# Performance work log

Hardware: AMD Instinct MI355X
Metric: run time of the kernel (lower is better)

The kernel has to match this reference:

```python
import jax, jax.numpy as jnp
import numpy as np

NH = 16  # num_heads from init_kwargs


def setup_inputs() -> dict:
    key = jax.random.key(0)
    ks = jax.random.split(key, 7)
    B, L, S, H = 4, 2, 1024, 1024
    s = 0.02  # weight init scale to keep logits numerically tame
    return {
        "x": jax.random.normal(ks[0], (B, S, H), jnp.float32),
        "y": jax.random.normal(ks[1], (L, B, S, H), jnp.float32),
        "bias": jax.random.normal(ks[2], (B, 1, 1, S), jnp.float32),
        "Wq": jax.random.normal(ks[3], (H, H), jnp.float32) * s,
        "Wk": jax.random.normal(ks[4], (L, H, H), jnp.float32) * s,
        "Wv": jax.random.normal(ks[5], (L, H, H), jnp.float32) * s,
        "Wo": jax.random.normal(ks[6], (H, H), jnp.float32) * s,
    }


def reference(x, y, bias, Wq, Wk, Wv, Wo):
    # x: [B, Lq, H]; y: [L, B, Lk, H] (stacked list of per-link memories)
    B, Lq, H = x.shape
    L, _, Lk, _ = y.shape
    d = H // NH

    # shared query projection, split heads: [B, NH, Lq, d], pre-scaled
    q = (x @ Wq).reshape(B, Lq, NH, d).transpose(0, 2, 1, 3) * (d ** -0.5)

    # per-link K/V projections, split heads -> [B, L, NH, Lk, d]
    kp = jnp.einsum('lbsh,lhe->lbse', y, Wk).reshape(L, B, Lk, NH, d).transpose(1, 0, 3, 2, 4)
    vp = jnp.einsum('lbsh,lhe->lbse', y, Wv).reshape(L, B, Lk, NH, d).transpose(1, 0, 3, 2, 4)

    # per-link logits [B, L, NH, Lq, Lk] + broadcast bias (concat across links == broadcast)
    logits = jnp.einsum('bhqd,blhkd->blhqk', q, kp) + bias[:, None]

    # computation_mode == 1: joint softmax over the link-summed logits
    joint = logits.sum(axis=1)                # [B, NH, Lq, Lk]
    w = jax.nn.softmax(joint, axis=-1)        # (training=False -> no dropout)

    # sum_l (w @ v_l) == w @ sum_l v_l  (w is shared across links)
    ctx = jnp.einsum('bhqk,bhkd->bhqd', w, vp.sum(axis=1))

    # combine heads [B, Lq, H] and output projection
    out = ctx.transpose(0, 2, 1, 3).reshape(B, Lq, H) @ Wo
    return out
```

## Files before the change

kernel.cpp:

```cpp
#include <hip/hip_runtime.h>
#include <cstdint>

typedef __bf16 bf16_t;
typedef bf16_t bf16x4 __attribute__((ext_vector_type(4)));
typedef bf16_t bf16x8 __attribute__((ext_vector_type(8)));
typedef float f32x4 __attribute__((ext_vector_type(4)));
typedef float f32x16 __attribute__((ext_vector_type(16)));

#define GLD_LDS16(g, l)                                                        \
  __builtin_amdgcn_global_load_lds(                                            \
      (const __attribute__((address_space(1))) void*)(g),                      \
      (__attribute__((address_space(3))) void*)(l), 16, 0, 0)

#define LOG2E 1.44269504088896340736f

static __device__ __forceinline__ unsigned short bf16_bits(float f) {
  bf16_t h = (bf16_t)f;
  return __builtin_bit_cast(unsigned short, h);
}

__global__ void prep_kernel(const float* __restrict__ x,
                            const float* __restrict__ y,
                            const float* __restrict__ Wq,
                            const float* __restrict__ Wk,
                            const float* __restrict__ Wv,
                            const float* __restrict__ Wo,
                            bf16_t* __restrict__ xb, bf16_t* __restrict__ yb,
                            bf16_t* __restrict__ WqT,
                            bf16_t* __restrict__ WkvT,
                            bf16_t* __restrict__ WoT) {
  __shared__ float tile[32][33];
  int bid = blockIdx.x;
  if (bid < 6144) {
    int i = bid * 256 + threadIdx.x;
    const float* src;
    bf16_t* dst;
    if (i < 524288) { src = x; dst = xb; }
    else            { src = y; dst = yb; i -= 524288; }
    const float4* s = (const float4*)src;
    float4 a = s[i * 2];
    float4 b = s[i * 2 + 1];
    bf16x8 o;
    o[0] = (bf16_t)a.x; o[1] = (bf16_t)a.y; o[2] = (bf16_t)a.z; o[3] = (bf16_t)a.w;
    o[4] = (bf16_t)b.x; o[5] = (bf16_t)b.y; o[6] = (bf16_t)b.z; o[7] = (bf16_t)b.w;
    *(bf16x8*)(dst + (size_t)i * 8) = o;
    return;
  }
  bid -= 6144;
  const float* src; bf16_t* dst; int R, lb;
  if (bid < 1024)      { src = Wq; dst = WqT;                        R = 1024; lb = bid; }
  else if (bid < 3072) { src = Wk; dst = WkvT;                       R = 2048; lb = bid - 1024; }
  else if (bid < 5120) { src = Wv; dst = WkvT + (size_t)1024 * 2048; R = 2048; lb = bid - 3072; }
  else                 { src = Wo; dst = WoT;                        R = 1024; lb = bid - 5120; }
  int c0 = (lb & 31) << 5, r0 = (lb >> 5) << 5;
  int tc = threadIdx.x & 31, tr = threadIdx.x >> 5;
#pragma unroll
  for (int i = 0; i < 4; i++)
    tile[tr + i * 8][tc] = src[(size_t)(r0 + tr + i * 8) * 1024 + c0 + tc];
  __syncthreads();
#pragma unroll
  for (int i = 0; i < 4; i++)
    dst[(size_t)(c0 + tr + i * 8) * R + r0 + tc] = (bf16_t)tile[tc][tr + i * 8];
}

#define GEMM_STAGE(buf, kt)                                                    \
  {                                                                            \
    const int kbase = (kt) * 32;                                               \
    int kg0 = kbase + ak0;                                                     \
    const bf16_t* s0 = (kg0 < Ksplit)                                          \
                           ? (A0 + (size_t)(m0 + ar0) * 1024 + kg0)            \
                           : (A1 + (size_t)(m0 + ar0) * 1024 + (kg0 - Ksplit));\
    GLD_LDS16(s0, As[buf] + c0 * 8);                                           \
    int kg1 = kbase + ak1;                                                     \
    const bf16_t* s1 = (kg1 < Ksplit)                                          \
                           ? (A0 + (size_t)(m0 + ar1) * 1024 + kg1)            \
                           : (A1 + (size_t)(m0 + ar1) * 1024 + (kg1 - Ksplit));\
    GLD_LDS16(s1, As[buf] + c1 * 8);                                           \
    const bf16_t* b0 = BT + (size_t)(n0 + ar0) * Ktot + kbase + ak0;           \
    GLD_LDS16(b0, Bs[buf] + c0 * 8);                                           \
    const bf16_t* b1 = BT + (size_t)(n0 + ar1) * Ktot + kbase + ak1;           \
    GLD_LDS16(b1, Bs[buf] + c1 * 8);                                           \
  }

#define GEMM_DECLS                                                             \
  const int t = threadIdx.x, w = t >> 6, l = t & 63;                           \
  const int l15 = l & 15, l4 = l >> 4;                                         \
  const int wr = w >> 1, wc = w & 1;                                           \
  const int c0 = t, c1 = t + 256;                                              \
  const int ar0 = c0 >> 2, ar1 = c1 >> 2;                                      \
  const int ak0 = ((c0 & 3) ^ ((ar0 >> 1) & 3)) * 8;                           \
  const int ak1 = ((c1 & 3) ^ ((ar1 >> 1) & 3)) * 8;                           \
  int offA[4], offB[4];                                                        \
  _Pragma("unroll") for (int mi = 0; mi < 4; mi++) {                           \
    int rA = wr * 64 + mi * 16 + l15;                                          \
    offA[mi] = rA * 32 + (l4 ^ ((rA >> 1) & 3)) * 8;                           \
    int rB = wc * 64 + mi * 16 + l15;                                          \
    offB[mi] = rB * 32 + (l4 ^ ((rB >> 1) & 3)) * 8;                           \
  }

#define GEMM_MAINLOOP                                                          \
  GEMM_STAGE(0, 0);                                                            \
  __syncthreads();                                                             \
  int cur = 0;                                                                 \
  for (int kt = 0; kt < nkt; ++kt) {                                           \
    if (kt + 1 < nkt) GEMM_STAGE(cur ^ 1, kt + 1);                             \
    bf16x8 af[4], bfr[4];                                                      \
    _Pragma("unroll") for (int mi = 0; mi < 4; mi++)                           \
        af[mi] = *(const bf16x8*)&As[cur][offA[mi]];                           \
    _Pragma("unroll") for (int ni = 0; ni < 4; ni++)                           \
        bfr[ni] = *(const bf16x8*)&Bs[cur][offB[ni]];                          \
    _Pragma("unroll") for (int mi = 0; mi < 4; mi++)                           \
        _Pragma("unroll") for (int ni = 0; ni < 4; ni++)                       \
            acc[mi][ni] = __builtin_amdgcn_mfma_f32_16x16x32_bf16(             \
                af[mi], bfr[ni], acc[mi][ni], 0, 0, 0);                        \
    __syncthreads();                                                           \
    cur ^= 1;                                                                  \
  }

__global__ __launch_bounds__(256, 2) void qkv_kernel(
    const bf16_t* __restrict__ xbp, const bf16_t* __restrict__ ybp,
    const bf16_t* __restrict__ WqT, const bf16_t* __restrict__ WkvT,
    bf16_t* __restrict__ Qb, bf16_t* __restrict__ Kb,
    bf16_t* __restrict__ VTb) {
  __shared__ bf16_t As[2][128 * 32];
  __shared__ bf16_t Bs[2][128 * 32];
  GEMM_DECLS
  const bool isQ = blockIdx.x < 256;
  const int i = isQ ? blockIdx.x : blockIdx.x - 256;
  const int ybt = (i & 7) * 4 + ((i >> 3) & 3);
  const int xbt = i >> 5;
  const int m0 = ybt * 128, n0 = xbt * 128;
  const bf16_t* A0 = isQ ? xbp : ybp;
  const bf16_t* A1 = isQ ? xbp : ybp + (size_t)4096 * 1024;
  const int Ksplit = 1024;
  const bf16_t* BT = isQ ? WqT : WkvT;
  const int Ktot = isQ ? 1024 : 2048;
  const int nkt = Ktot >> 5;
  f32x4 acc[4][4] = {};

  GEMM_MAINLOOP

#pragma unroll
  for (int mi = 0; mi < 4; mi++) {
#pragma unroll
    for (int ni = 0; ni < 4; ni++) {
      const int rbase = m0 + wr * 64 + mi * 16 + l4 * 4;
      const int col = n0 + wc * 64 + ni * 16 + l15;
      if (isQ) {
#pragma unroll
        for (int rr = 0; rr < 4; rr++)
          Qb[(size_t)(rbase + rr) * 1024 + col] =
              (bf16_t)(acc[mi][ni][rr] * (0.125f * LOG2E));
      } else if (n0 < 1024) {
#pragma unroll
        for (int rr = 0; rr < 4; rr++)
          Kb[(size_t)(rbase + rr) * 1024 + col] = (bf16_t)acc[mi][ni][rr];
      } else {
        union { unsigned short u[4]; uint2 v; } pk;
#pragma unroll
        for (int rr = 0; rr < 4; rr++)
          pk.u[rr] = bf16_bits(acc[mi][ni][rr]);
        *(uint2*)&VTb[(size_t)(col - 1024) * 4096 + rbase] = pk.v;
      }
    }
  }
}

__global__ __launch_bounds__(256, 2) void gemm_o(const bf16_t* __restrict__ A0,
                                                 const bf16_t* __restrict__ BT,
                                                 float* __restrict__ Cp) {
  __shared__ bf16_t As[2][128 * 32];
  __shared__ bf16_t Bs[2][64 * 32];
  const int t = threadIdx.x, w = t >> 6, l = t & 63;
  const int l15 = l & 15, l4 = l >> 4;
  const int wr = w >> 1, wc = w & 1;
  const int c0 = t, c1 = t + 256, c2 = t;
  const int ar0 = c0 >> 2, ar1 = c1 >> 2, br2 = c2 >> 2;
  const int ak0 = ((c0 & 3) ^ ((ar0 >> 1) & 3)) * 8;
  const int ak1 = ((c1 & 3) ^ ((ar1 >> 1) & 3)) * 8;
  const int bk2 = ((c2 & 3) ^ ((br2 >> 1) & 3)) * 8;
  int offA[4], offB[2];
#pragma unroll
  for (int mi = 0; mi < 4; mi++) {
    int rA = wr * 64 + mi * 16 + l15;
    offA[mi] = rA * 32 + (l4 ^ ((rA >> 1) & 3)) * 8;
  }
#pragma unroll
  for (int ni = 0; ni < 2; ni++) {
    int rB = wc * 32 + ni * 16 + l15;
    offB[ni] = rB * 32 + (l4 ^ ((rB >> 1) & 3)) * 8;
  }
  const int i = blockIdx.x;
  const int ybt = (i & 7) * 4 + ((i >> 3) & 3);
  const int xbt = i >> 5;
  const int m0 = ybt * 128, n0 = xbt * 64;
  const int nkt = 32;
  f32x4 acc[4][2] = {};

#define OST(buf, kt)                                                           \
  {                                                                            \
    const int kbase = (kt) * 32;                                               \
    const bf16_t* s0 = A0 + (size_t)(m0 + ar0) * 1024 + kbase + ak0;           \
    GLD_LDS16(s0, As[buf] + c0 * 8);                                           \
    const bf16_t* s1 = A0 + (size_t)(m0 + ar1) * 1024 + kbase + ak1;           \
    GLD_LDS16(s1, As[buf] + c1 * 8);                                           \
    const bf16_t* b0 = BT + (size_t)(n0 + br2) * 1024 + kbase + bk2;           \
    GLD_LDS16(b0, Bs[buf] + c2 * 8);                                           \
  }

  OST(0, 0);
  __syncthreads();
  int cur = 0;
  for (int kt = 0; kt < nkt; ++kt) {
    if (kt + 1 < nkt) OST(cur ^ 1, kt + 1);
    bf16x8 af[4], bfr[2];
#pragma unroll
    for (int mi = 0; mi < 4; mi++)
      af[mi] = *(const bf16x8*)&As[cur][offA[mi]];
#pragma unroll
    for (int ni = 0; ni < 2; ni++)
      bfr[ni] = *(const bf16x8*)&Bs[cur][offB[ni]];
#pragma unroll
    for (int mi = 0; mi < 4; mi++)
#pragma unroll
      for (int ni = 0; ni < 2; ni++)
        acc[mi][ni] = __builtin_amdgcn_mfma_f32_16x16x32_bf16(
            af[mi], bfr[ni], acc[mi][ni], 0, 0, 0);
    __syncthreads();
    cur ^= 1;
  }
#undef OST

#pragma unroll
  for (int mi = 0; mi < 4; mi++) {
#pragma unroll
    for (int ni = 0; ni < 2; ni++) {
      const int rbase = m0 + wr * 64 + mi * 16 + l4 * 4;
      const int col = n0 + wc * 32 + ni * 16 + l15;
#pragma unroll
      for (int rr = 0; rr < 4; rr++)
        Cp[(size_t)(rbase + rr) * 1024 + col] = acc[mi][ni][rr];
    }
  }
}

__global__ __launch_bounds__(256, 2) void attn_kernel(
    const bf16_t* __restrict__ Q, const bf16_t* __restrict__ K,
    const bf16_t* __restrict__ VT, const float* __restrict__ bias,
    bf16_t* __restrict__ ctx) {
  __shared__ bf16_t Ks[2][128 * 64];
  __shared__ bf16_t Vs[2][64 * 128];
  const int t = threadIdx.x, w = t >> 6, l = t & 63;
  const int l31 = l & 31, hi = l >> 5;
  const int id = blockIdx.x;
  const int bh = id & 63, qt = id >> 6;
  const int b = bh >> 4, h = bh & 15;
  const int q_local = w * 32 + l31;

  bf16x8 qf[4];
  {
    const bf16_t* Qp =
        Q + (size_t)(b * 1024 + qt * 128 + q_local) * 1024 + h * 64 + hi * 8;
#pragma unroll
    for (int ds = 0; ds < 4; ds++) qf[ds] = *(const bf16x8*)&Qp[ds * 16];
  }

#define ATTN_STAGE(buf, kt)                                                    \
  {                                                                            \
    _Pragma("unroll") for (int j = 0; j < 4; j++) {                            \
      int c = t + j * 256;                                                     \
      int rowk = c >> 3, slk = (c & 7) ^ (rowk & 7);                           \
      const bf16_t* srck =                                                     \
          K + (size_t)(b * 1024 + (kt) * 128 + rowk) * 1024 + h * 64 + slk * 8;\
      GLD_LDS16(srck, Ks[buf] + c * 8);                                        \
      int rowv = c >> 4, slv = (c & 15) ^ ((rowv & 7) << 1);                   \
      const bf16_t* srcv =                                                     \
          VT + (size_t)(h * 64 + rowv) * 4096 + b * 1024 + (kt) * 128 +        \
          slv * 8;                                                             \
      GLD_LDS16(srcv, Vs[buf] + c * 8);                                        \
    }                                                                          \
  }

  float mrun = -INFINITY, lrun = 0.f;
  f32x16 cacc[2] = {};

  ATTN_STAGE(0, 0);
  __syncthreads();
  int cur = 0;
  for (int kts = 0; kts < 8; ++kts) {
    if (kts + 1 < 8) ATTN_STAGE(cur ^ 1, kts + 1);

#pragma unroll
    for (int half = 0; half < 2; ++half) {
      f32x16 sacc[2] = {};
#pragma unroll
      for (int ds = 0; ds < 4; ds++) {
#pragma unroll
        for (int kg = 0; kg < 2; kg++) {
          int krow = half * 64 + kg * 32 + l31;
          int eoff = krow * 64 + (((ds * 2 + hi) ^ (krow & 7)) * 8);
          bf16x8 kf = *(const bf16x8*)&Ks[cur][eoff];
          sacc[kg] = __builtin_amdgcn_mfma_f32_32x32x16_bf16(
              kf, qf[ds], sacc[kg], 0, 0, 0);
        }
      }
#pragma unroll
      for (int kg = 0; kg < 2; kg++) {
#pragma unroll
        for (int mm = 0; mm < 4; mm++) {
          f32x4 bb = *(const f32x4*)&bias[b * 1024 + kts * 128 + half * 64 +
                                          kg * 32 + mm * 8 + hi * 4];
#pragma unroll
          for (int rr = 0; rr < 4; rr++)
            sacc[kg][mm * 4 + rr] += (2.0f * LOG2E) * bb[rr];
        }
      }
      float tm = -INFINITY;
#pragma unroll
      for (int kg = 0; kg < 2; kg++)
#pragma unroll
        for (int r = 0; r < 16; r++) tm = fmaxf(tm, sacc[kg][r]);
      tm = fmaxf(tm, __shfl_xor(tm, 32));
      float mnew = fmaxf(mrun, tm);
      float sc = exp2f(mrun - mnew);
      float rsum = 0.f;
#pragma unroll
      for (int kg = 0; kg < 2; kg++)
#pragma unroll
        for (int r = 0; r < 16; r++) {
          float p = exp2f(sacc[kg][r] - mnew);
          sacc[kg][r] = p;
          rsum += p;
        }
      rsum += __shfl_xor(rsum, 32);
      lrun = lrun * sc + rsum;
      mrun = mnew;
#pragma unroll
      for (int dg = 0; dg < 2; dg++)
#pragma unroll
        for (int r = 0; r < 16; r++) cacc[dg][r] *= sc;

      bf16x8 pb[4];
#pragma unroll
      for (int kg = 0; kg < 2; kg++) {
#pragma unroll
        for (int tt = 0; tt < 2; tt++) {
          uint32_t w0A, w1A, w0B, w1B;
          const int mA = 2 * tt, mB = 2 * tt + 1;
          asm("v_cvt_pk_bf16_f32 %0, %1, %2"
              : "=v"(w0A)
              : "v"(sacc[kg][4 * mA + 0]), "v"(sacc[kg][4 * mA + 1]));
          asm("v_cvt_pk_bf16_f32 %0, %1, %2"
              : "=v"(w1A)
              : "v"(sacc[kg][4 * mA + 2]), "v"(sacc[kg][4 * mA + 3]));
          asm("v_cvt_pk_bf16_f32 %0, %1, %2"
              : "=v"(w0B)
              : "v"(sacc[kg][4 * mB + 0]), "v"(sacc[kg][4 * mB + 1]));
          asm("v_cvt_pk_bf16_f32 %0, %1, %2"
              : "=v"(w1B)
              : "v"(sacc[kg][4 * mB + 2]), "v"(sacc[kg][4 * mB + 3]));
          asm("v_permlane32_swap_b32 %0, %1" : "+v"(w0A), "+v"(w0B));
          asm("v_permlane32_swap_b32 %0, %1" : "+v"(w1A), "+v"(w1B));
          union { uint32_t u[4]; bf16x8 v; } pk;
          pk.u[0] = w0A; pk.u[1] = w1A; pk.u[2] = w0B; pk.u[3] = w1B;
          pb[kg * 2 + tt] = pk.v;
        }
      }
#pragma unroll
      for (int dg = 0; dg < 2; dg++) {
#pragma unroll
        for (int k4 = 0; k4 < 4; k4++) {
          int vrow = dg * 32 + l31;
          int s = half * 8 + k4 * 2 + hi;
          int eoff = vrow * 128 + ((s ^ ((vrow & 7) << 1)) * 8);
          bf16x8 vf = *(const bf16x8*)&Vs[cur][eoff];
          cacc[dg] = __builtin_amdgcn_mfma_f32_32x32x16_bf16(
              vf, pb[k4], cacc[dg], 0, 0, 0);
        }
      }
    }
    __syncthreads();
    cur ^= 1;
  }

  bf16_t* T = (bf16_t*)Ks;
  {
    float inv = 1.0f / lrun;
#pragma unroll
    for (int dg = 0; dg < 2; dg++) {
#pragma unroll
      for (int m = 0; m < 4; m++) {
        bf16x4 tv;
#pragma unroll
        for (int rr = 0; rr < 4; rr++)
          tv[rr] = (bf16_t)(cacc[dg][4 * m + rr] * inv);
        int d0 = dg * 32 + m * 8 + hi * 4;
        *(bf16x4*)&T[q_local * 64 + (d0 ^ ((q_local & 7) << 3))] = tv;
      }
    }
  }
  __syncthreads();
#pragma unroll
  for (int c = t; c < 1024; c += 256) {
    int row = c >> 3, col8 = c & 7;
    bf16x8 v = *(const bf16x8*)&T[row * 64 + ((col8 * 8) ^ ((row & 7) << 3))];
    *(bf16x8*)&ctx[(size_t)(b * 1024 + qt * 128 + row) * 1024 + h * 64 +
                   col8 * 8] = v;
  }
#undef ATTN_STAGE
}

extern "C" void kernel_launch(void* const* d_in, const int* in_sizes, int n_in,
                              void* d_out, int out_size, void* d_ws,
                              size_t ws_size, hipStream_t stream) {
  const float* x = (const float*)d_in[0];
  const float* y = (const float*)d_in[1];
  const float* bias = (const float*)d_in[2];
  const float* Wq = (const float*)d_in[3];
  const float* Wk = (const float*)d_in[4];
  const float* Wv = (const float*)d_in[5];
  const float* Wo = (const float*)d_in[6];
  float* out = (float*)d_out;

  char* ws = (char*)d_ws;
  const size_t MB = 1024 * 1024;
  bf16_t* xb   = (bf16_t*)(ws + 0 * MB);
  bf16_t* yb   = (bf16_t*)(ws + 8 * MB);
  bf16_t* WqT  = (bf16_t*)(ws + 24 * MB);
  bf16_t* WkvT = (bf16_t*)(ws + 26 * MB);
  bf16_t* WoT  = (bf16_t*)(ws + 34 * MB);
  bf16_t* Qb   = (bf16_t*)(ws + 36 * MB);
  bf16_t* Kb   = (bf16_t*)(ws + 44 * MB);
  bf16_t* VTb  = (bf16_t*)(ws + 52 * MB);
  bf16_t* ctxb = (bf16_t*)(ws + 60 * MB);

  prep_kernel<<<12288, 256, 0, stream>>>(x, y, Wq, Wk, Wv, Wo, xb, yb, WqT,
                                         WkvT, WoT);
  qkv_kernel<<<768, 256, 0, stream>>>(xb, yb, WqT, WkvT, Qb, Kb, VTb);
  attn_kernel<<<512, 256, 0, stream>>>(Qb, Kb, VTb, bias, ctxb);
  gemm_o<<<512, 256, 0, stream>>>(ctxb, WoT, out);
}
```

Before: 134.3 us.

## Fuse fp32-to-bf16 activation conversion into QKV GEMM A-operand loads

Removes the separate pass that converts x and y from fp32 to bf16. The QKV GEMM now reads fp32 activations straight into registers, converts them, and writes them into swizzled LDS, with a register-staged prefetch of the next k-tile. The block order is also changed so the K/V blocks launch before the Q blocks. This avoids writing and rereading roughly 24MB of bf16 intermediates, at the cost of twice the global A-operand bytes inside the GEMM and a full vmcnt(0) wait each iteration that may limit overlap.

```diff
diff --git a/kernel.cpp b/kernel.cpp
--- a/kernel.cpp
+++ b/kernel.cpp
@@ -19,34 +19,15 @@
   return __builtin_bit_cast(unsigned short, h);
 }
 
-__global__ void prep_kernel(const float* __restrict__ x,
-                            const float* __restrict__ y,
-                            const float* __restrict__ Wq,
+__global__ void prep_kernel(const float* __restrict__ Wq,
                             const float* __restrict__ Wk,
                             const float* __restrict__ Wv,
                             const float* __restrict__ Wo,
-                            bf16_t* __restrict__ xb, bf16_t* __restrict__ yb,
                             bf16_t* __restrict__ WqT,
                             bf16_t* __restrict__ WkvT,
                             bf16_t* __restrict__ WoT) {
   __shared__ float tile[32][33];
   int bid = blockIdx.x;
-  if (bid < 6144) {
-    int i = bid * 256 + threadIdx.x;
-    const float* src;
-    bf16_t* dst;
-    if (i < 524288) { src = x; dst = xb; }
-    else            { src = y; dst = yb; i -= 524288; }
-    const float4* s = (const float4*)src;
-    float4 a = s[i * 2];
-    float4 b = s[i * 2 + 1];
-    bf16x8 o;
-    o[0] = (bf16_t)a.x; o[1] = (bf16_t)a.y; o[2] = (bf16_t)a.z; o[3] = (bf16_t)a.w;
-    o[4] = (bf16_t)b.x; o[5] = (bf16_t)b.y; o[6] = (bf16_t)b.z; o[7] = (bf16_t)b.w;
-    *(bf16x8*)(dst + (size_t)i * 8) = o;
-    return;
-  }
-  bid -= 6144;
   const float* src; bf16_t* dst; int R, lb;
   if (bid < 1024)      { src = Wq; dst = WqT;                        R = 1024; lb = bid; }
   else if (bid < 3072) { src = Wk; dst = WkvT;                       R = 2048; lb = bid - 1024; }
@@ -63,82 +44,109 @@
     dst[(size_t)(c0 + tr + i * 8) * R + r0 + tc] = (bf16_t)tile[tc][tr + i * 8];
 }
 
-#define GEMM_STAGE(buf, kt)                                                    \
-  {                                                                            \
-    const int kbase = (kt) * 32;                                               \
-    int kg0 = kbase + ak0;                                                     \
-    const bf16_t* s0 = (kg0 < Ksplit)                                          \
-                           ? (A0 + (size_t)(m0 + ar0) * 1024 + kg0)            \
-                           : (A1 + (size_t)(m0 + ar0) * 1024 + (kg0 - Ksplit));\
-    GLD_LDS16(s0, As[buf] + c0 * 8);                                           \
-    int kg1 = kbase + ak1;                                                     \
-    const bf16_t* s1 = (kg1 < Ksplit)                                          \
-                           ? (A0 + (size_t)(m0 + ar1) * 1024 + kg1)            \
-                           : (A1 + (size_t)(m0 + ar1) * 1024 + (kg1 - Ksplit));\
-    GLD_LDS16(s1, As[buf] + c1 * 8);                                           \
-    const bf16_t* b0 = BT + (size_t)(n0 + ar0) * Ktot + kbase + ak0;           \
-    GLD_LDS16(b0, Bs[buf] + c0 * 8);                                           \
-    const bf16_t* b1 = BT + (size_t)(n0 + ar1) * Ktot + kbase + ak1;           \
-    GLD_LDS16(b1, Bs[buf] + c1 * 8);                                           \
-  }
-
-#define GEMM_DECLS                                                             \
-  const int t = threadIdx.x, w = t >> 6, l = t & 63;                           \
-  const int l15 = l & 15, l4 = l >> 4;                                         \
-  const int wr = w >> 1, wc = w & 1;                                           \
-  const int c0 = t, c1 = t + 256;                                              \
-  const int ar0 = c0 >> 2, ar1 = c1 >> 2;                                      \
-  const int ak0 = ((c0 & 3) ^ ((ar0 >> 1) & 3)) * 8;                           \
-  const int ak1 = ((c1 & 3) ^ ((ar1 >> 1) & 3)) * 8;                           \
-  int offA[4], offB[4];                                                        \
-  _Pragma("unroll") for (int mi = 0; mi < 4; mi++) {                           \
-    int rA = wr * 64 + mi * 16 + l15;                                          \
-    offA[mi] = rA * 32 + (l4 ^ ((rA >> 1) & 3)) * 8;                           \
-    int rB = wc * 64 + mi * 16 + l15;                                          \
-    offB[mi] = rB * 32 + (l4 ^ ((rB >> 1) & 3)) * 8;                           \
-  }
-
-#define GEMM_MAINLOOP                                                          \
-  GEMM_STAGE(0, 0);                                                            \
-  __syncthreads();                                                             \
-  int cur = 0;                                                                 \
-  for (int kt = 0; kt < nkt; ++kt) {                                           \
-    if (kt + 1 < nkt) GEMM_STAGE(cur ^ 1, kt + 1);                             \
-    bf16x8 af[4], bfr[4];                                                      \
-    _Pragma("unroll") for (int mi = 0; mi < 4; mi++)                           \
-        af[mi] = *(const bf16x8*)&As[cur][offA[mi]];                           \
-    _Pragma("unroll") for (int ni = 0; ni < 4; ni++)                           \
-        bfr[ni] = *(const bf16x8*)&Bs[cur][offB[ni]];                          \
-    _Pragma("unroll") for (int mi = 0; mi < 4; mi++)                           \
-        _Pragma("unroll") for (int ni = 0; ni < 4; ni++)                       \
-            acc[mi][ni] = __builtin_amdgcn_mfma_f32_16x16x32_bf16(             \
-                af[mi], bfr[ni], acc[mi][ni], 0, 0, 0);                        \
-    __syncthreads();                                                           \
-    cur ^= 1;                                                                  \
-  }
-
 __global__ __launch_bounds__(256, 2) void qkv_kernel(
-    const bf16_t* __restrict__ xbp, const bf16_t* __restrict__ ybp,
+    const float* __restrict__ xf, const float* __restrict__ yf,
     const bf16_t* __restrict__ WqT, const bf16_t* __restrict__ WkvT,
     bf16_t* __restrict__ Qb, bf16_t* __restrict__ Kb,
     bf16_t* __restrict__ VTb) {
   __shared__ bf16_t As[2][128 * 32];
   __shared__ bf16_t Bs[2][128 * 32];
-  GEMM_DECLS
-  const bool isQ = blockIdx.x < 256;
-  const int i = isQ ? blockIdx.x : blockIdx.x - 256;
+  const int t = threadIdx.x, w = t >> 6, l = t & 63;
+  const int l15 = l & 15, l4 = l >> 4;
+  const int wr = w >> 1, wc = w & 1;
+  const int c0 = t, c1 = t + 256;
+  const int br0 = c0 >> 2, br1 = c1 >> 2;
+  const int bk0 = ((c0 & 3) ^ ((br0 >> 1) & 3)) * 8;
+  const int bk1 = ((c1 & 3) ^ ((br1 >> 1) & 3)) * 8;
+  const int ar = t >> 1, ac = (t & 1) * 16;
+  const int sw = (ar >> 1) & 3, sbase = (t & 1) * 2;
+  const int woff0 = ar * 32 + ((sbase) ^ sw) * 8;
+  const int woff1 = ar * 32 + ((sbase + 1) ^ sw) * 8;
+  int offA[4], offB[4];
+#pragma unroll
+  for (int mi = 0; mi < 4; mi++) {
+    int rA = wr * 64 + mi * 16 + l15;
+    offA[mi] = rA * 32 + (l4 ^ ((rA >> 1) & 3)) * 8;
+    int rB = wc * 64 + mi * 16 + l15;
+    offB[mi] = rB * 32 + (l4 ^ ((rB >> 1) & 3)) * 8;
+  }
+  const bool isQ = blockIdx.x >= 512;
+  const int i = isQ ? blockIdx.x - 512 : blockIdx.x;
   const int ybt = (i & 7) * 4 + ((i >> 3) & 3);
   const int xbt = i >> 5;
   const int m0 = ybt * 128, n0 = xbt * 128;
-  const bf16_t* A0 = isQ ? xbp : ybp;
-  const bf16_t* A1 = isQ ? xbp : ybp + (size_t)4096 * 1024;
-  const int Ksplit = 1024;
+  const float* A0f = isQ ? xf : yf;
+  const float* A1f = isQ ? xf : yf + (size_t)4096 * 1024;
   const bf16_t* BT = isQ ? WqT : WkvT;
   const int Ktot = isQ ? 1024 : 2048;
   const int nkt = Ktot >> 5;
   f32x4 acc[4][4] = {};
-
-  GEMM_MAINLOOP
+  float4 areg[4];
+
+#define LOAD_A(kt)                                                             \
+  {                                                                            \
+    const int kb = (kt) * 32 + ac;                                             \
+    _Pragma("unroll") for (int j = 0; j < 4; j++) {                            \
+      int kg = kb + j * 4;                                                     \
+      const float* src = (kg < 1024)                                           \
+                             ? (A0f + (size_t)(m0 + ar) * 1024 + kg)           \
+                             : (A1f + (size_t)(m0 + ar) * 1024 + (kg - 1024)); \
+      areg[j] = *(const float4*)src;                                           \
+    }                                                                          \
+  }
+#define STAGE_B(buf, kt)                                                       \
+  {                                                                            \
+    const int kb = (kt) * 32;                                                  \
+    GLD_LDS16(BT + (size_t)(n0 + br0) * Ktot + kb + bk0, Bs[buf] + c0 * 8);    \
+    GLD_LDS16(BT + (size_t)(n0 + br1) * Ktot + kb + bk1, Bs[buf] + c1 * 8);    \
+  }
+#define WRITE_A(buf)                                                           \
+  {                                                                            \
+    bf16x8 ch0, ch1;                                                           \
+    ch0[0] = (bf16_t)areg[0].x; ch0[1] = (bf16_t)areg[0].y;                    \
+    ch0[2] = (bf16_t)areg[0].z; ch0[3] = (bf16_t)areg[0].w;                    \
+    ch0[4] = (bf16_t)areg[1].x; ch0[5] = (bf16_t)areg[1].y;                    \
+    ch0[6] = (bf16_t)areg[1].z; ch0[7] = (bf16_t)areg[1].w;                    \
+    ch1[0] = (bf16_t)areg[2].x; ch1[1] = (bf16_t)areg[2].y;                    \
+    ch1[2] = (bf16_t)areg[2].z; ch1[3] = (bf16_t)areg[2].w;                    \
+    ch1[4] = (bf16_t)areg[3].x; ch1[5] = (bf16_t)areg[3].y;                    \
+    ch1[6] = (bf16_t)areg[3].z; ch1[7] = (bf16_t)areg[3].w;                    \
+    *(bf16x8*)&As[buf][woff0] = ch0;                                           \
+    *(bf16x8*)&As[buf][woff1] = ch1;                                           \
+  }
+
+  LOAD_A(0);
+  STAGE_B(0, 0);
+  asm volatile("s_waitcnt vmcnt(0)" ::: "memory");
+  WRITE_A(0);
+  __syncthreads();
+  int cur = 0;
+  for (int kt = 0; kt < nkt; ++kt) {
+    const bool more = (kt + 1 < nkt);
+    if (more) { LOAD_A(kt + 1); STAGE_B(cur ^ 1, kt + 1); }
+    bf16x8 af[4], bfr[4];
+#pragma unroll
+    for (int mi = 0; mi < 4; mi++)
+      af[mi] = *(const bf16x8*)&As[cur][offA[mi]];
+#pragma unroll
+    for (int ni = 0; ni < 4; ni++)
+      bfr[ni] = *(const bf16x8*)&Bs[cur][offB[ni]];
+#pragma unroll
+    for (int mi = 0; mi < 4; mi++)
+#pragma unroll
+      for (int ni = 0; ni < 4; ni++)
+        acc[mi][ni] = __builtin_amdgcn_mfma_f32_16x16x32_bf16(
+            af[mi], bfr[ni], acc[mi][ni], 0, 0, 0);
+    if (more) {
+      asm volatile("s_waitcnt vmcnt(0)" ::: "memory");
+      WRITE_A(cur ^ 1);
+    }
+    __syncthreads();
+    cur ^= 1;
+  }
+#undef LOAD_A
+#undef STAGE_B
+#undef WRITE_A
 
 #pragma unroll
   for (int mi = 0; mi < 4; mi++) {
@@ -424,19 +432,16 @@
 
   char* ws = (char*)d_ws;
   const size_t MB = 1024 * 1024;
-  bf16_t* xb   = (bf16_t*)(ws + 0 * MB);
-  bf16_t* yb   = (bf16_t*)(ws + 8 * MB);
-  bf16_t* WqT  = (bf16_t*)(ws + 24 * MB);
-  bf16_t* WkvT = (bf16_t*)(ws + 26 * MB);
-  bf16_t* WoT  = (bf16_t*)(ws + 34 * MB);
-  bf16_t* Qb   = (bf16_t*)(ws + 36 * MB);
-  bf16_t* Kb   = (bf16_t*)(ws + 44 * MB);
-  bf16_t* VTb  = (bf16_t*)(ws + 52 * MB);
-  bf16_t* ctxb = (bf16_t*)(ws + 60 * MB);
-
-  prep_kernel<<<12288, 256, 0, stream>>>(x, y, Wq, Wk, Wv, Wo, xb, yb, WqT,
-                                         WkvT, WoT);
-  qkv_kernel<<<768, 256, 0, stream>>>(xb, yb, WqT, WkvT, Qb, Kb, VTb);
+  bf16_t* WqT  = (bf16_t*)(ws + 0 * MB);
+  bf16_t* WkvT = (bf16_t*)(ws + 2 * MB);
+  bf16_t* WoT  = (bf16_t*)(ws + 10 * MB);
+  bf16_t* Qb   = (bf16_t*)(ws + 12 * MB);
+  bf16_t* Kb   = (bf16_t*)(ws + 20 * MB);
+  bf16_t* VTb  = (bf16_t*)(ws + 28 * MB);
+  bf16_t* ctxb = (bf16_t*)(ws + 36 * MB);
+
+  prep_kernel<<<6144, 256, 0, stream>>>(Wq, Wk, Wv, Wo, WqT, WkvT, WoT);
+  qkv_kernel<<<768, 256, 0, stream>>>(x, y, WqT, WkvT, Qb, Kb, VTb);
   attn_kernel<<<512, 256, 0, stream>>>(Qb, Kb, VTb, bias, ctxb);
   gemm_o<<<512, 256, 0, stream>>>(ctxb, WoT, out);
 }
```

Result: slower. 142.5 us (+6.1%).
